# Optimization experiments

Measured on AMD Instinct MI355X. Metric: run time of the kernel, lower is better.

The kernel has to match this reference:

```python
import jax, jax.numpy as jnp
import numpy as np

# NF4 codebook (bitsandbytes nf4 data type, 16 levels)
NF4_TABLE = np.array([
    -1.0, -0.6961928009986877, -0.5250730514526367, -0.39491748809814453,
    -0.28444138169288635, -0.18477343022823334, -0.09105003625154495, 0.0,
    0.07958029955625534, 0.16093020141124725, 0.24611230194568634,
    0.33791524171829224, 0.44070982933044434, 0.5626170039176941,
    0.7229568362236023, 1.0], dtype=np.float32)

BLOCKSIZE = 64
SCALING = 32.0 / 16.0  # lora_alpha / r


def setup_inputs() -> dict:
    key = jax.random.key(0)
    k1, k2, k3, k4, k5 = jax.random.split(key, 5)
    tokens, in_f, out_f, r = 256, 4096, 11008, 16
    x = jax.random.normal(k1, (tokens, in_f), dtype=jnp.float32)
    q_codes = jax.random.randint(k2, (out_f, in_f), 0, 16, dtype=jnp.int32)
    absmax = jax.random.uniform(k3, (out_f, in_f // BLOCKSIZE), dtype=jnp.float32)
    lora_A = jax.random.normal(k4, (r, in_f), dtype=jnp.float32) * (1.0 / np.sqrt(in_f))
    lora_B = jax.random.normal(k5, (out_f, r), dtype=jnp.float32) * 0.02
    return {"x": x, "q_codes": q_codes, "absmax": absmax,
            "lora_A": lora_A, "lora_B": lora_B}


def reference(x, q_codes, absmax, lora_A, lora_B):
    out_f, in_f = q_codes.shape
    nf4 = jnp.asarray(NF4_TABLE, dtype=x.dtype)
    # Dequantize: codebook lookup, then per-block absmax scale.
    W = nf4[q_codes].reshape(out_f, in_f // BLOCKSIZE, BLOCKSIZE)
    W = (W * absmax[:, :, None]).reshape(out_f, in_f)  # [out_f, in_f]
    # Base 4-bit linear (no bias in bnb Linear4bit default here).
    base = x @ W.T  # [tokens, out_f]
    # LoRA path: dropout p=0 is identity in eval; scaling = alpha/r.
    lora = (x @ lora_A.T) @ lora_B.T  # [tokens, r] -> [tokens, out_f]
    return base + lora * jnp.asarray(SCALING, dtype=x.dtype)
```

## Files before the change

kernel.cpp:

```cpp
#include <hip/hip_runtime.h>
#include <hip/hip_fp16.h>

typedef unsigned int uint;
typedef unsigned short ushort;

typedef __attribute__((ext_vector_type(8))) _Float16 f16x8;
typedef __attribute__((ext_vector_type(4))) float f32x4;

#define TOK 256
#define OUTF 11008
#define INF 4096
#define BM 256
#define BN 64
#define NT2 172
#define CVT_BLKS 2048
#define KSPLIT 4

__device__ __constant__ float NF4_TBL[16] = {
    -1.0f, -0.6961928009986877f, -0.5250730514526367f, -0.39491748809814453f,
    -0.28444138169288635f, -0.18477343022823334f, -0.09105003625154495f, 0.0f,
    0.07958029955625534f, 0.16093020141124725f, 0.24611230194568634f,
    0.33791524171829224f, 0.44070982933044434f, 0.5626170039176941f,
    0.7229568362236023f, 1.0f};

__device__ __forceinline__ ushort f2h(float f) {
  return __half_as_ushort(__float2half(f));
}

__device__ __forceinline__ void async_cp16(const void* g, void* l) {
  __builtin_amdgcn_global_load_lds(
      (const __attribute__((address_space(1))) uint*)g,
      (__attribute__((address_space(3))) uint*)l, 16, 0, 0);
}

__device__ __forceinline__ float nf4v(int c, int tbits) {
  return __int_as_float(__builtin_amdgcn_ds_bpermute(c << 2, tbits));
}

__device__ __forceinline__ uint2 dq4(int4 c, __half2 ax2, int tbits) {
  __half2 h0 = __floats2half2_rn(nf4v(c.x, tbits), nf4v(c.y, tbits));
  __half2 h1 = __floats2half2_rn(nf4v(c.z, tbits), nf4v(c.w, tbits));
  h0 = __hmul2(h0, ax2);
  h1 = __hmul2(h1, ax2);
  union { __half2 h[2]; uint2 u; } r;
  r.h[0] = h0; r.h[1] = h1;
  return r.u;
}

__global__ __launch_bounds__(256)
void prep_kernel(const float4* __restrict__ x4, ushort4* __restrict__ xh4,
                 const float4* __restrict__ lB4, ushort4* __restrict__ lBh4,
                 const float* __restrict__ x, const float* __restrict__ lA,
                 ushort* __restrict__ xa2, float4* __restrict__ out4) {
  if (blockIdx.x < CVT_BLKS) {
    const int stride = CVT_BLKS * blockDim.x;
    const int t0 = blockIdx.x * blockDim.x + threadIdx.x;
    for (int i = t0; i < TOK * INF / 4; i += stride) {
      float4 v = x4[i];
      ushort4 o;
      o.x = f2h(v.x); o.y = f2h(v.y); o.z = f2h(v.z); o.w = f2h(v.w);
      xh4[i] = o;
    }
    for (int i = t0; i < OUTF * 16; i += stride) {
      int n = i >> 4, jq = i & 15;
      ushort4 o = {0, 0, 0, 0};
      if (jq < 4) {
        float4 v = lB4[n * 4 + jq];
        o.x = f2h(v.x); o.y = f2h(v.y); o.z = f2h(v.z); o.w = f2h(v.w);
      }
      lBh4[i] = o;
    }
    const float4 z = {0.f, 0.f, 0.f, 0.f};
    for (int i = t0; i < TOK * OUTF / 4; i += stride) out4[i] = z;
  } else {
    const int m = blockIdx.x - CVT_BLKS;
    const int t = threadIdx.x;
    const float4* xm4 = (const float4*)(x + (size_t)m * INF);
    const float4* lA4 = (const float4*)lA;
    float4 xv[4];
#pragma unroll
    for (int c = 0; c < 4; ++c) xv[c] = xm4[c * 256 + t];
    float acc[16];
#pragma unroll
    for (int j = 0; j < 16; ++j) {
      acc[j] = 0.f;
#pragma unroll
      for (int c = 0; c < 4; ++c) {
        float4 a = lA4[j * (INF / 4) + c * 256 + t];
        acc[j] += xv[c].x * a.x + xv[c].y * a.y + xv[c].z * a.z + xv[c].w * a.w;
      }
    }
#pragma unroll
    for (int j = 0; j < 16; ++j)
#pragma unroll
      for (int s = 32; s > 0; s >>= 1) acc[j] += __shfl_xor(acc[j], s, 64);
    __shared__ float red[4][16];
    const int w = t >> 6, l = t & 63;
    if (l == 0) {
#pragma unroll
      for (int j = 0; j < 16; ++j) red[w][j] = acc[j];
    }
    __syncthreads();
    if (t < 64) {
      ushort v = 0;
      if (t < 16) {
        float s = red[0][t] + red[1][t] + red[2][t] + red[3][t];
        v = f2h(2.0f * s);
      }
      xa2[m * 64 + t] = v;
    }
  }
}

__global__ __launch_bounds__(256, 3)
void gemm_kernel(const int* __restrict__ qc, const float* __restrict__ am,
                 const ushort* __restrict__ xh, const ushort* __restrict__ lBh,
                 const ushort* __restrict__ xa2, float* __restrict__ out, int nst) {
  __shared__ ushort Abuf[BM * 64];
  __shared__ ushort Bbuf[64 * 64];
  __shared__ float Qax[1024];

  const int tid = threadIdx.x;
  const int w = tid >> 6;
  const int l = tid & 63;
  const int chunk = l >> 4;
  const int rlo = l & 15;
  const int split = blockIdx.x / NT2;
  const int ntile = blockIdx.x - split * NT2;
  const int n0 = ntile * BN;
  const int kb0 = split * nst;

  const int tbits = __float_as_int(NF4_TBL[l & 15]);

  const int arow = w * 8 + (l >> 3);
  const int acol = ((l & 7) ^ (l >> 3)) << 3;
  int aoff[2][4];
#pragma unroll
  for (int ks2 = 0; ks2 < 2; ++ks2) {
    const int cc = ks2 * 4 + chunk;
#pragma unroll
    for (int mt = 0; mt < 4; ++mt)
      aoff[ks2][mt] = (w * 64 + mt * 16 + rlo) * 64 + ((cc ^ (l & 7)) << 3);
  }

  const int qrg = tid >> 4;
  const int qch = tid & 15;
  const int* qbase[4];
  int bdst[4];
#pragma unroll
  for (int p = 0; p < 4; ++p) {
    int r = p * 16 + qrg;
    qbase[p] = qc + (size_t)(n0 + r) * INF + kb0 * 64 + qch * 4;
    bdst[p] = r * 64 + (((qch >> 1) ^ (r & 7)) << 3) + (qch & 1) * 4;
  }

  int boff[2][4];
#pragma unroll
  for (int ks2 = 0; ks2 < 2; ++ks2)
#pragma unroll
    for (int nt = 0; nt < 4; ++nt)
      boff[ks2][nt] = (nt * 16 + rlo) * 64 + (((ks2 * 4 + chunk) ^ (rlo & 7)) << 3);

  f32x4 acc[4][4];
#pragma unroll
  for (int mt = 0; mt < 4; ++mt)
#pragma unroll
    for (int nt = 0; nt < 4; ++nt) acc[mt][nt] = (f32x4){0.f, 0.f, 0.f, 0.f};

  if (w == 0) {
#pragma unroll
    for (int j = 0; j < 4; ++j)
      async_cp16(am + (size_t)(n0 + l) * 64 + kb0 + j * 4, (char*)Qax + j * 1024);
  }
#pragma unroll
  for (int i = 0; i < 8; ++i) {
    const ushort* g = xh + (size_t)(i * 32 + arow) * INF + kb0 * 64 + acol;
    async_cp16(g, &Abuf[(i * 256 + w * 64) * 8]);
  }
  int4 qreg[2][4];
#pragma unroll
  for (int p = 0; p < 4; ++p) qreg[0][p] = *(const int4*)(qbase[p]);

  for (int s = 0; s < nst; ++s) {
    const int par = s & 1;
    __syncthreads();

    if (s + 1 < nst) {
#pragma unroll
      for (int p = 0; p < 4; ++p)
        qreg[par ^ 1][p] = *(const int4*)(qbase[p] + (s + 1) * 64);
    }

    const int sl = s & 15;
#pragma unroll
    for (int p = 0; p < 4; ++p) {
      int r = p * 16 + qrg;
      __half2 ax2 = __float2half2_rn(Qax[(sl >> 2) * 256 + r * 4 + (sl & 3)]);
      *(uint2*)&Bbuf[bdst[p]] = dq4(qreg[par][p], ax2, tbits);
    }
    f16x8 areg[2][4];
#pragma unroll
    for (int ks2 = 0; ks2 < 2; ++ks2)
#pragma unroll
      for (int mt = 0; mt < 4; ++mt) areg[ks2][mt] = *(const f16x8*)&Abuf[aoff[ks2][mt]];

    __syncthreads();

    if (s + 1 < nst) {
      const int kb = kb0 + s + 1;
#pragma unroll
      for (int i = 0; i < 8; ++i) {
        const ushort* g = xh + (size_t)(i * 32 + arow) * INF + kb * 64 + acol;
        async_cp16(g, &Abuf[(i * 256 + w * 64) * 8]);
      }
    }

#pragma unroll
    for (int ks2 = 0; ks2 < 2; ++ks2) {
      f16x8 b[4];
#pragma unroll
      for (int nt = 0; nt < 4; ++nt) b[nt] = *(const f16x8*)&Bbuf[boff[ks2][nt]];
#pragma unroll
      for (int mt = 0; mt < 4; ++mt)
#pragma unroll
        for (int nt = 0; nt < 4; ++nt)
          acc[mt][nt] = __builtin_amdgcn_mfma_f32_16x16x32_f16(areg[ks2][mt], b[nt], acc[mt][nt], 0, 0, 0);
    }
  }

  if (split == 0) {
    f16x8 a_l[4], b_l[4];
#pragma unroll
    for (int mt = 0; mt < 4; ++mt)
      a_l[mt] = *(const f16x8*)(xa2 + (size_t)(w * 64 + mt * 16 + rlo) * 64 + chunk * 8);
#pragma unroll
    for (int nt = 0; nt < 4; ++nt)
      b_l[nt] = *(const f16x8*)(lBh + (size_t)(n0 + nt * 16 + rlo) * 64 + chunk * 8);
#pragma unroll
    for (int mt = 0; mt < 4; ++mt)
#pragma unroll
      for (int nt = 0; nt < 4; ++nt)
        acc[mt][nt] = __builtin_amdgcn_mfma_f32_16x16x32_f16(a_l[mt], b_l[nt], acc[mt][nt], 0, 0, 0);
  }

#pragma unroll
  for (int mt = 0; mt < 4; ++mt) {
#pragma unroll
    for (int nt = 0; nt < 4; ++nt) {
      int c = n0 + nt * 16 + rlo;
#pragma unroll
      for (int r = 0; r < 4; ++r) {
        int row = w * 64 + mt * 16 + chunk * 4 + r;
        unsafeAtomicAdd(&out[(size_t)row * OUTF + c], acc[mt][nt][r]);
      }
    }
  }
}

extern "C" void kernel_launch(void* const* d_in, const int* in_sizes, int n_in,
                              void* d_out, int out_size, void* d_ws, size_t ws_size,
                              hipStream_t stream) {
  const float* x = (const float*)d_in[0];
  const int* qc = (const int*)d_in[1];
  const float* am = (const float*)d_in[2];
  const float* lA = (const float*)d_in[3];
  const float* lB = (const float*)d_in[4];
  float* out = (float*)d_out;

  const size_t off_lB = (size_t)TOK * INF * 2;
  const size_t off_xa2 = off_lB + (size_t)OUTF * 64 * 2;
  ushort* xh = (ushort*)d_ws;
  ushort* lBh = (ushort*)((char*)d_ws + off_lB);
  ushort* xa2 = (ushort*)((char*)d_ws + off_xa2);

  prep_kernel<<<CVT_BLKS + TOK, 256, 0, stream>>>(
      (const float4*)x, (ushort4*)xh, (const float4*)lB, (ushort4*)lBh,
      x, lA, xa2, (float4*)out);
  gemm_kernel<<<NT2 * KSPLIT, 256, 0, stream>>>(qc, am, xh, lBh, xa2, out, 64 / KSPLIT);
}
```

Measured before the change: 349.5 us.

## Replace split-K atomic accumulation with partial buffers and a separate reduce kernel

Each K-split block now writes its partial tile with plain stores into a per-split workspace buffer instead of issuing atomic adds into the output. A new reduce kernel sums the four partials into the output, and the output zero-fill in the prep kernel is removed. This avoids atomic read-modify-write traffic and contention on the output. In exchange it adds a larger workspace, extra global memory reads and writes, and an additional kernel launch.

```diff
diff --git a/kernel.cpp b/kernel.cpp
--- a/kernel.cpp
+++ b/kernel.cpp
@@ -51,7 +51,7 @@
 void prep_kernel(const float4* __restrict__ x4, ushort4* __restrict__ xh4,
                  const float4* __restrict__ lB4, ushort4* __restrict__ lBh4,
                  const float* __restrict__ x, const float* __restrict__ lA,
-                 ushort* __restrict__ xa2, float4* __restrict__ out4) {
+                 ushort* __restrict__ xa2) {
   if (blockIdx.x < CVT_BLKS) {
     const int stride = CVT_BLKS * blockDim.x;
     const int t0 = blockIdx.x * blockDim.x + threadIdx.x;
@@ -70,8 +70,6 @@
       }
       lBh4[i] = o;
     }
-    const float4 z = {0.f, 0.f, 0.f, 0.f};
-    for (int i = t0; i < TOK * OUTF / 4; i += stride) out4[i] = z;
   } else {
     const int m = blockIdx.x - CVT_BLKS;
     const int t = threadIdx.x;
@@ -115,7 +113,7 @@
 __global__ __launch_bounds__(256, 3)
 void gemm_kernel(const int* __restrict__ qc, const float* __restrict__ am,
                  const ushort* __restrict__ xh, const ushort* __restrict__ lBh,
-                 const ushort* __restrict__ xa2, float* __restrict__ out, int nst) {
+                 const ushort* __restrict__ xa2, float* __restrict__ dest, int nst) {
   __shared__ ushort Abuf[BM * 64];
   __shared__ ushort Bbuf[64 * 64];
   __shared__ float Qax[1024];
@@ -243,6 +241,7 @@
         acc[mt][nt] = __builtin_amdgcn_mfma_f32_16x16x32_f16(a_l[mt], b_l[nt], acc[mt][nt], 0, 0, 0);
   }
 
+  float* dst = dest + (size_t)split * TOK * OUTF;
 #pragma unroll
   for (int mt = 0; mt < 4; ++mt) {
 #pragma unroll
@@ -251,9 +250,23 @@
 #pragma unroll
       for (int r = 0; r < 4; ++r) {
         int row = w * 64 + mt * 16 + chunk * 4 + r;
-        unsafeAtomicAdd(&out[(size_t)row * OUTF + c], acc[mt][nt][r]);
-      }
-    }
+        dst[(size_t)row * OUTF + c] = acc[mt][nt][r];
+      }
+    }
+  }
+}
+
+__global__ void reduce_kernel(const float4* __restrict__ part, float4* __restrict__ out) {
+  const int QN = TOK * OUTF / 4;
+  int i = blockIdx.x * blockDim.x + threadIdx.x;
+  if (i < QN) {
+    float4 s = part[i];
+#pragma unroll
+    for (int s2 = 1; s2 < KSPLIT; ++s2) {
+      float4 p = part[(size_t)s2 * QN + i];
+      s.x += p.x; s.y += p.y; s.z += p.z; s.w += p.w;
+    }
+    out[i] = s;
   }
 }
 
@@ -269,12 +282,16 @@
 
   const size_t off_lB = (size_t)TOK * INF * 2;
   const size_t off_xa2 = off_lB + (size_t)OUTF * 64 * 2;
+  const size_t off_part = off_xa2 + (size_t)TOK * 64 * 2;
+
   ushort* xh = (ushort*)d_ws;
   ushort* lBh = (ushort*)((char*)d_ws + off_lB);
   ushort* xa2 = (ushort*)((char*)d_ws + off_xa2);
+  float* part = (float*)((char*)d_ws + off_part);
 
   prep_kernel<<<CVT_BLKS + TOK, 256, 0, stream>>>(
-      (const float4*)x, (ushort4*)xh, (const float4*)lB, (ushort4*)lBh,
-      x, lA, xa2, (float4*)out);
-  gemm_kernel<<<NT2 * KSPLIT, 256, 0, stream>>>(qc, am, xh, lBh, xa2, out, 64 / KSPLIT);
-}
+      (const float4*)x, (ushort4*)xh, (const float4*)lB, (ushort4*)lBh, x, lA, xa2);
+  gemm_kernel<<<NT2 * KSPLIT, 256, 0, stream>>>(qc, am, xh, lBh, xa2, part, 64 / KSPLIT);
+  reduce_kernel<<<(TOK * OUTF / 4 + 255) / 256, 256, 0, stream>>>((const float4*)part,
+                                                                  (float4*)out);
+}
```

After: 346.4 us. Within noise of the previous version (-0.9%).
